# Kernel optimization log

Measured on AMD Instinct MI355X. Metric: run time of the kernel, lower is better.

The kernel has to match this reference:

```python
import jax, jax.numpy as jnp
import numpy as np

B, N = 4, 1024
IN_FEAT = 64
FNET = 64          # code requires fnet_feat == in_feat
OUT_FEAT = 64
RANK = 16
ST1 = 16
ST2 = 16
MIN_NN = 16


def _roll_idx(n_rolls, stride, F):
    # myroll(h, shift) == roll right by `shift` (mod F). Shifts used: 0, then (ss+1)*stride for ss=1..n_rolls-1.
    shifts = np.array([0] + [(ss + 1) * stride for ss in range(1, n_rolls)])
    j = np.arange(F)
    return jnp.asarray((j[None, :] - shifts[:, None]) % F)  # [n_rolls, F]


def setup_inputs() -> dict:
    key = jax.random.key(0)
    ks = jax.random.split(key, 10)
    h = jax.random.normal(ks[0], (B, N, IN_FEAT), jnp.float32)
    D = jax.random.uniform(ks[1], (B, N, N), jnp.float32)
    W0 = jax.random.normal(ks[2], (IN_FEAT, FNET), jnp.float32) * (1.0 / np.sqrt(IN_FEAT))
    b0 = jax.random.normal(ks[3], (1, FNET), jnp.float32) * 0.02
    W1 = jax.random.normal(ks[4], (FNET, ST1 * RANK), jnp.float32) * (1.0 / (np.sqrt(FNET) * np.sqrt(IN_FEAT)))
    b1 = jax.random.normal(ks[5], (1, RANK, IN_FEAT), jnp.float32) * 0.02
    W2 = jax.random.normal(ks[6], (FNET, ST2 * RANK), jnp.float32) * (1.0 / (np.sqrt(FNET) * np.sqrt(IN_FEAT)))
    b2 = jax.random.normal(ks[7], (1, RANK, OUT_FEAT), jnp.float32) * 0.02
    Wl = jax.random.normal(ks[8], (FNET, RANK), jnp.float32) * (1.0 / np.sqrt(RANK))
    bl = jax.random.normal(ks[9], (1, RANK), jnp.float32) * 0.02
    return {"h": h, "D": D, "W0": W0, "b0": b0, "W1": W1, "b1": b1,
            "W2": W2, "b2": b2, "Wl": Wl, "bl": bl}


def reference(h, D, W0, b0, W1, b1, W2, b2, Wl, bl):
    Bb, Nn, f = h.shape
    # k+1 nearest (smallest D): index 0 is the closest ('self'), 1..k are the neighbors
    _, top_idx = jax.lax.top_k(-D, MIN_NN + 1)            # [B, N, K+1]
    top_idx2 = jnp.repeat(top_idx[:, :, 0], MIN_NN, axis=1)  # [B, N*K] (repeat_interleave)
    nbr = top_idx[:, :, 1:].reshape(Bb, Nn * MIN_NN)         # [B, N*K]
    xt1 = jnp.take_along_axis(h, nbr[:, :, None], axis=1)    # [B, N*K, f]
    xt2 = jnp.take_along_axis(h, top_idx2[:, :, None], axis=1)
    labels = (xt1 - xt2).reshape(-1, f)                      # [E, f], E = B*N*K
    x1 = xt1.reshape(-1, f)
    d_labels = jnp.sum(labels * labels, axis=1).reshape(-1, MIN_NN)  # [B*N, K]
    lab = jax.nn.leaky_relu(labels @ W0 + b0, negative_slope=0.02)   # [E, FNET]
    E = lab.shape[0]
    idx1 = _roll_idx(IN_FEAT // ST1, ST1, FNET)
    idx2 = _roll_idx(OUT_FEAT // ST2, ST2, FNET)
    # per-edge weight generation via rolled copies of lab
    theta1 = (lab[:, idx1].reshape(-1, FNET) @ W1).reshape(E, RANK, IN_FEAT) + b1   # [E, R, in]
    theta2 = (lab[:, idx2].reshape(-1, FNET) @ W2).reshape(E, RANK, OUT_FEAT) + b2  # [E, R, out]
    thetal = lab @ Wl + bl                                                          # [E, R]
    x = jnp.einsum('erf,ef->er', theta1, x1) * thetal      # [E, R]
    x = jnp.einsum('ero,er->eo', theta2, x)                # [E, out]
    x = x.reshape(-1, MIN_NN, OUT_FEAT) * jnp.exp(-d_labels / 10.0)[:, :, None]
    x = jnp.sum(x, axis=1).reshape(-1, OUT_FEAT, Nn)       # faithful to torch .reshape(-1, out, N)
    return x
```

## Files before the change

kernel.cpp:

```cpp
#include <hip/hip_runtime.h>
#include <math.h>

#define NN 1024
#define K 16

typedef _Float16 f16;
typedef f16 f16x8 __attribute__((ext_vector_type(8)));
typedef float f32x4 __attribute__((ext_vector_type(4)));

#define W0F_OFF 0
#define W1F_OFF 8192
#define W2F_OFF 40960
#define WLF_OFF 73728
#define B1F_OFF 75776
#define FRAG_BYTES 77824

#define MFMA16(a,b,c) __builtin_amdgcn_mfma_f32_16x16x32_f16((a),(b),(c),0,0,0)

template<int CTRL>
__device__ __forceinline__ float dppf(float v) {
    return __int_as_float(__builtin_amdgcn_update_dpp(0, __float_as_int(v), CTRL, 0xF, 0xF, true));
}
__device__ __forceinline__ float rowsum16(float v) {
    v += dppf<0xB1>(v);
    v += dppf<0x4E>(v);
    v += dppf<0x124>(v);
    v += dppf<0x128>(v);
    return v;
}

__global__ __launch_bounds__(256) void pre_kernel(const float* __restrict__ D,
                                                  const float* __restrict__ W0,
                                                  const float* __restrict__ W1,
                                                  const float* __restrict__ W2,
                                                  const float* __restrict__ Wl,
                                                  const float* __restrict__ b1,
                                                  int* __restrict__ selfIdx,
                                                  int* __restrict__ nbrIdx,
                                                  f16* __restrict__ frag) {
    if (blockIdx.x >= 1024) {
        int c = (blockIdx.x - 1024) * 256 + threadIdx.x;
        if (c >= 76 * 64) return;
        int fg   = c >> 6;
        int lane = c & 63;
        int lrow = lane & 15;
        int kgrp = lane >> 4;
        float src[8];
        if (fg < 8) {
            int kt = fg >> 2, nt = fg & 3;
            int n = nt * 16 + lrow;
#pragma unroll
            for (int i = 0; i < 8; ++i) src[i] = W0[(kt * 32 + kgrp * 8 + i) * 64 + n];
        } else if (fg < 40) {
            int t = fg - 8;
            int q = t >> 3, kt = (t >> 2) & 1, nt = t & 3;
            int f = nt * 16 + lrow;
#pragma unroll
            for (int i = 0; i < 8; ++i) src[i] = W1[f * 256 + q * 64 + kt * 32 + kgrp * 8 + i];
        } else if (fg < 72) {
            int t = fg - 40;
            int q = t >> 3, kt = (t >> 2) & 1, nt = t & 3;
            int o = nt * 16 + lrow;
#pragma unroll
            for (int i = 0; i < 8; ++i) src[i] = W2[(kt * 32 + kgrp * 8 + i) * 256 + q * 64 + o];
        } else if (fg < 74) {
            int kt = fg - 72;
#pragma unroll
            for (int i = 0; i < 8; ++i) src[i] = Wl[(kt * 32 + kgrp * 8 + i) * 16 + lrow];
        } else {
            int kt = fg - 74;
#pragma unroll
            for (int i = 0; i < 8; ++i) src[i] = b1[lrow * 64 + kt * 32 + kgrp * 8 + i];
        }
        f16x8 v;
#pragma unroll
        for (int i = 0; i < 8; ++i) v[i] = (f16)src[i];
        *(f16x8*)((unsigned char*)frag + fg * 1024 + lane * 16) = v;
        return;
    }

    int row  = blockIdx.x * 4 + (threadIdx.x >> 6);
    int lane = threadIdx.x & 63;
    const float* Drow = D + (size_t)row * NN;

    float v[16];
#pragma unroll
    for (int j = 0; j < 16; ++j) v[j] = Drow[j * 64 + lane];

    for (int t = 0; t < K + 1; ++t) {
        float bv = v[0]; int bj = 0;
#pragma unroll
        for (int j = 1; j < 16; ++j)
            if (v[j] < bv) { bv = v[j]; bj = j; }
        int bidx = bj * 64 + lane;
#pragma unroll
        for (int off = 32; off > 0; off >>= 1) {
            float ov = __shfl_xor(bv, off);
            int   oi = __shfl_xor(bidx, off);
            if (ov < bv || (ov == bv && oi < bidx)) { bv = ov; bidx = oi; }
        }
        if (lane == 0) {
            if (t == 0) selfIdx[row] = bidx;
            else        nbrIdx[row * K + (t - 1)] = bidx;
        }
        if ((bidx & 63) == lane) v[bidx >> 6] = INFINITY;
    }
}

__global__ __launch_bounds__(1024, 1) void node_kernel(
    const float* __restrict__ h,
    const float* __restrict__ b0, const float* __restrict__ b2,
    const float* __restrict__ bl,
    const f16* __restrict__ frag,
    const int* __restrict__ selfIdx, const int* __restrict__ nbrIdx,
    float* __restrict__ out) {

    __shared__ __attribute__((aligned(16))) unsigned char sfrag[FRAG_BYTES];
    __shared__ __attribute__((aligned(16))) f16 sbuf[16 * 1152];

    const int tid  = threadIdx.x;
    const int wid  = tid >> 6;
    const int lane = tid & 63;
    const int lrow = lane & 15;
    const int kgrp = lane >> 4;

    {
        const f16x8* gsrc = (const f16x8*)frag;
        f16x8* ldst = (f16x8*)sfrag;
#pragma unroll
        for (int it = 0; it < 5; ++it) {
            int c = tid + it * 1024;
            if (c < FRAG_BYTES / 16) ldst[c] = gsrc[c];
        }
    }
    __syncthreads();

    const unsigned char* fb = sfrag;
    f16* buf = sbuf + wid * 1152;
    const int node = blockIdx.x * 16 + wid;

    const float* hb = h + ((size_t)(node >> 10) << 16);
    const int self = selfIdx[node];
    const int nb   = nbrIdx[node * 16 + lrow];

    f16x8 x1f[2], lrf[2];
    float dp = 0.f;
#pragma unroll
    for (int kt = 0; kt < 2; ++kt) {
        const float* p1 = hb + nb * 64 + kt * 32 + kgrp * 8;
        const float* p2 = hb + self * 64 + kt * 32 + kgrp * 8;
        float4 a0 = *(const float4*)(p1);
        float4 a1 = *(const float4*)(p1 + 4);
        float4 s0 = *(const float4*)(p2);
        float4 s1 = *(const float4*)(p2 + 4);
        float xs[8] = {a0.x,a0.y,a0.z,a0.w,a1.x,a1.y,a1.z,a1.w};
        float ss[8] = {s0.x,s0.y,s0.z,s0.w,s1.x,s1.y,s1.z,s1.w};
#pragma unroll
        for (int i = 0; i < 8; ++i) {
            float t = xs[i] - ss[i];
            x1f[kt][i] = (f16)xs[i];
            lrf[kt][i] = (f16)t;
            dp = fmaf(t, t, dp);
        }
    }
    dp += __shfl_xor(dp, 16);
    dp += __shfl_xor(dp, 32);
    const float dv = dp;

    f32x4 labf[4];
#pragma unroll
    for (int nt = 0; nt < 4; ++nt) {
        float bb = b0[nt * 16 + lrow];
        labf[nt] = (f32x4){bb, bb, bb, bb};
    }
#pragma unroll
    for (int kt = 0; kt < 2; ++kt)
#pragma unroll
        for (int nt = 0; nt < 4; ++nt) {
            f16x8 bf = *(const f16x8*)(fb + W0F_OFF + (kt * 4 + nt) * 1024 + lane * 16);
            labf[nt] = MFMA16(lrf[kt], bf, labf[nt]);
        }
#pragma unroll
    for (int nt = 0; nt < 4; ++nt)
#pragma unroll
        for (int j = 0; j < 4; ++j) {
            float v = labf[nt][j];
            v = v > 0.f ? v : 0.02f * v;
            labf[nt][j] = v;
            buf[(kgrp*4 + j) * 72 + nt*16 + lrow] = (f16)v;
        }

    f32x4 thlf, b1xf;
    {
        float blv = bl[lrow];
        thlf = (f32x4){blv, blv, blv, blv};
        b1xf = (f32x4){0.f, 0.f, 0.f, 0.f};
#pragma unroll
        for (int kt = 0; kt < 2; ++kt) {
            f16x8 wl = *(const f16x8*)(fb + WLF_OFF + kt * 1024 + lane * 16);
            f16x8 bb = *(const f16x8*)(fb + B1F_OFF + kt * 1024 + lane * 16);
            f16x8 la = *(const f16x8*)&buf[lrow * 72 + kt*32 + kgrp*8];
            thlf = MFMA16(la, wl, thlf);
            b1xf = MFMA16(x1f[kt], bb, b1xf);
        }
    }

    f32x4 xof[4];
#pragma unroll
    for (int nt = 0; nt < 4; ++nt) xof[nt] = (f32x4){0.f, 0.f, 0.f, 0.f};

#pragma unroll
    for (int q = 0; q < 4; ++q) {
        f32x4 Uf[4];
#pragma unroll
        for (int nt = 0; nt < 4; ++nt) Uf[nt] = (f32x4){0.f, 0.f, 0.f, 0.f};
#pragma unroll
        for (int kt = 0; kt < 2; ++kt)
#pragma unroll
            for (int nt = 0; nt < 4; ++nt) {
                f16x8 bf = *(const f16x8*)(fb + W1F_OFF + (q*8 + kt*4 + nt) * 1024 + lane * 16);
                Uf[nt] = MFMA16(x1f[kt], bf, Uf[nt]);
            }

        f32x4 dsv[3];
#pragma unroll
        for (int si = 0; si < 3; ++si) {
            const int ts = (si == 0) ? 0 : (si == 1) ? 2 : 3;
            f32x4 p = labf[0] * Uf[(0 + ts) & 3];
            p += labf[1] * Uf[(1 + ts) & 3];
            p += labf[2] * Uf[(2 + ts) & 3];
            p += labf[3] * Uf[(3 + ts) & 3];
#pragma unroll
            for (int j = 0; j < 4; ++j) p[j] = rowsum16(p[j]);
            dsv[si] = p;
        }

        f32x4 xr[4];
#pragma unroll
        for (int p = 0; p < 4; ++p) {
            const int si = (p == 1) ? 1 : (p == 2) ? 2 : 0;
            f32x4 cand = (dsv[si] + b1xf) * thlf;
            int srcl = (lane & 48) | (p * 4 + q);
#pragma unroll
            for (int j = 0; j < 4; ++j) xr[p][j] = __shfl(cand[j], srcl);
        }

        {
            f32x4 x03 = xr[0] + xr[3];
#pragma unroll
            for (int nt = 0; nt < 4; ++nt) {
                f32x4 v = labf[nt] * x03
                        + labf[(nt + 2) & 3] * xr[1]
                        + labf[(nt + 1) & 3] * xr[2];
#pragma unroll
                for (int j = 0; j < 4; ++j)
                    buf[(kgrp*4 + j) * 72 + nt*16 + lrow] = (f16)v[j];
            }
        }

#pragma unroll
        for (int kt = 0; kt < 2; ++kt) {
            f16x8 av = *(const f16x8*)&buf[lrow * 72 + kt*32 + kgrp*8];
#pragma unroll
            for (int nt = 0; nt < 4; ++nt) {
                f16x8 bf = *(const f16x8*)(fb + W2F_OFF + (q*8 + kt*4 + nt) * 1024 + lane * 16);
                xof[nt] = MFMA16(av, bf, xof[nt]);
            }
        }

#pragma unroll
        for (int p = 0; p < 4; ++p)
#pragma unroll
            for (int nt = 0; nt < 4; ++nt) {
                float bv = b2[(p*4 + q) * 64 + nt*16 + lrow];
                xof[nt] += xr[p] * bv;
            }
    }

    f32x4 ew;
#pragma unroll
    for (int j = 0; j < 4; ++j) {
        float dd = __shfl(dv, kgrp * 4 + j);
        ew[j] = __expf(-dd * 0.1f);
    }
    float cs[4];
#pragma unroll
    for (int nt = 0; nt < 4; ++nt) {
        f32x4 wp = xof[nt] * ew;
        float s = wp[0] + wp[1] + wp[2] + wp[3];
        s += __shfl_xor(s, 16);
        s += __shfl_xor(s, 32);
        cs[nt] = s;
    }
    float v = (kgrp == 0) ? cs[0] : (kgrp == 1) ? cs[1] : (kgrp == 2) ? cs[2] : cs[3];
    out[(size_t)node * 64 + lane] = v;
}

extern "C" void kernel_launch(void* const* d_in, const int* in_sizes, int n_in,
                              void* d_out, int out_size, void* d_ws, size_t ws_size,
                              hipStream_t stream) {
    const float* h  = (const float*)d_in[0];
    const float* D  = (const float*)d_in[1];
    const float* W0 = (const float*)d_in[2];
    const float* b0 = (const float*)d_in[3];
    const float* W1 = (const float*)d_in[4];
    const float* b1 = (const float*)d_in[5];
    const float* W2 = (const float*)d_in[6];
    const float* b2 = (const float*)d_in[7];
    const float* Wl = (const float*)d_in[8];
    const float* bl = (const float*)d_in[9];
    float* out = (float*)d_out;

    int* selfIdx = (int*)d_ws;
    int* nbrIdx  = selfIdx + 4096;
    f16* frag    = (f16*)(nbrIdx + 65536);

    pre_kernel<<<1043, 256, 0, stream>>>(D, W0, W1, W2, Wl, b1,
                                         selfIdx, nbrIdx, frag);
    node_kernel<<<256, 1024, 0, stream>>>(h, b0, b2, bl, frag,
                                          selfIdx, nbrIdx, out);
}
```

Measured before the change: 40.52 us.

## Fuse top-k neighbor selection into node kernel and overlap fragment staging

Moves the per-row top-17 search over D from the pre-kernel into the node kernel, so each wave finds its own self and neighbor indices in registers instead of writing them to global memory and reading them back. The weight-fragment global loads are issued into registers before the top-k work and written to shared memory afterward, hiding their latency. The prep kernel now only builds weight fragments with 19 blocks. In exchange, the top-k runs on only 256 blocks of 1024 threads at one block per CU, which lowers parallelism for the D scan.

```diff
diff --git a/kernel.cpp b/kernel.cpp
--- a/kernel.cpp
+++ b/kernel.cpp
@@ -29,90 +29,56 @@
     return v;
 }
 
-__global__ __launch_bounds__(256) void pre_kernel(const float* __restrict__ D,
-                                                  const float* __restrict__ W0,
-                                                  const float* __restrict__ W1,
-                                                  const float* __restrict__ W2,
-                                                  const float* __restrict__ Wl,
-                                                  const float* __restrict__ b1,
-                                                  int* __restrict__ selfIdx,
-                                                  int* __restrict__ nbrIdx,
-                                                  f16* __restrict__ frag) {
-    if (blockIdx.x >= 1024) {
-        int c = (blockIdx.x - 1024) * 256 + threadIdx.x;
-        if (c >= 76 * 64) return;
-        int fg   = c >> 6;
-        int lane = c & 63;
-        int lrow = lane & 15;
-        int kgrp = lane >> 4;
-        float src[8];
-        if (fg < 8) {
-            int kt = fg >> 2, nt = fg & 3;
-            int n = nt * 16 + lrow;
-#pragma unroll
-            for (int i = 0; i < 8; ++i) src[i] = W0[(kt * 32 + kgrp * 8 + i) * 64 + n];
-        } else if (fg < 40) {
-            int t = fg - 8;
-            int q = t >> 3, kt = (t >> 2) & 1, nt = t & 3;
-            int f = nt * 16 + lrow;
-#pragma unroll
-            for (int i = 0; i < 8; ++i) src[i] = W1[f * 256 + q * 64 + kt * 32 + kgrp * 8 + i];
-        } else if (fg < 72) {
-            int t = fg - 40;
-            int q = t >> 3, kt = (t >> 2) & 1, nt = t & 3;
-            int o = nt * 16 + lrow;
-#pragma unroll
-            for (int i = 0; i < 8; ++i) src[i] = W2[(kt * 32 + kgrp * 8 + i) * 256 + q * 64 + o];
-        } else if (fg < 74) {
-            int kt = fg - 72;
-#pragma unroll
-            for (int i = 0; i < 8; ++i) src[i] = Wl[(kt * 32 + kgrp * 8 + i) * 16 + lrow];
-        } else {
-            int kt = fg - 74;
-#pragma unroll
-            for (int i = 0; i < 8; ++i) src[i] = b1[lrow * 64 + kt * 32 + kgrp * 8 + i];
-        }
-        f16x8 v;
-#pragma unroll
-        for (int i = 0; i < 8; ++i) v[i] = (f16)src[i];
-        *(f16x8*)((unsigned char*)frag + fg * 1024 + lane * 16) = v;
-        return;
-    }
-
-    int row  = blockIdx.x * 4 + (threadIdx.x >> 6);
-    int lane = threadIdx.x & 63;
-    const float* Drow = D + (size_t)row * NN;
-
-    float v[16];
-#pragma unroll
-    for (int j = 0; j < 16; ++j) v[j] = Drow[j * 64 + lane];
-
-    for (int t = 0; t < K + 1; ++t) {
-        float bv = v[0]; int bj = 0;
-#pragma unroll
-        for (int j = 1; j < 16; ++j)
-            if (v[j] < bv) { bv = v[j]; bj = j; }
-        int bidx = bj * 64 + lane;
-#pragma unroll
-        for (int off = 32; off > 0; off >>= 1) {
-            float ov = __shfl_xor(bv, off);
-            int   oi = __shfl_xor(bidx, off);
-            if (ov < bv || (ov == bv && oi < bidx)) { bv = ov; bidx = oi; }
-        }
-        if (lane == 0) {
-            if (t == 0) selfIdx[row] = bidx;
-            else        nbrIdx[row * K + (t - 1)] = bidx;
-        }
-        if ((bidx & 63) == lane) v[bidx >> 6] = INFINITY;
-    }
+__global__ __launch_bounds__(256) void prep_kernel(const float* __restrict__ W0,
+                                                   const float* __restrict__ W1,
+                                                   const float* __restrict__ W2,
+                                                   const float* __restrict__ Wl,
+                                                   const float* __restrict__ b1,
+                                                   f16* __restrict__ frag) {
+    int c = blockIdx.x * 256 + threadIdx.x;
+    if (c >= 76 * 64) return;
+    int fg   = c >> 6;
+    int lane = c & 63;
+    int lrow = lane & 15;
+    int kgrp = lane >> 4;
+    float src[8];
+    if (fg < 8) {
+        int kt = fg >> 2, nt = fg & 3;
+        int n = nt * 16 + lrow;
+#pragma unroll
+        for (int i = 0; i < 8; ++i) src[i] = W0[(kt * 32 + kgrp * 8 + i) * 64 + n];
+    } else if (fg < 40) {
+        int t = fg - 8;
+        int q = t >> 3, kt = (t >> 2) & 1, nt = t & 3;
+        int f = nt * 16 + lrow;
+#pragma unroll
+        for (int i = 0; i < 8; ++i) src[i] = W1[f * 256 + q * 64 + kt * 32 + kgrp * 8 + i];
+    } else if (fg < 72) {
+        int t = fg - 40;
+        int q = t >> 3, kt = (t >> 2) & 1, nt = t & 3;
+        int o = nt * 16 + lrow;
+#pragma unroll
+        for (int i = 0; i < 8; ++i) src[i] = W2[(kt * 32 + kgrp * 8 + i) * 256 + q * 64 + o];
+    } else if (fg < 74) {
+        int kt = fg - 72;
+#pragma unroll
+        for (int i = 0; i < 8; ++i) src[i] = Wl[(kt * 32 + kgrp * 8 + i) * 16 + lrow];
+    } else {
+        int kt = fg - 74;
+#pragma unroll
+        for (int i = 0; i < 8; ++i) src[i] = b1[lrow * 64 + kt * 32 + kgrp * 8 + i];
+    }
+    f16x8 v;
+#pragma unroll
+    for (int i = 0; i < 8; ++i) v[i] = (f16)src[i];
+    *(f16x8*)((unsigned char*)frag + fg * 1024 + lane * 16) = v;
 }
 
 __global__ __launch_bounds__(1024, 1) void node_kernel(
-    const float* __restrict__ h,
+    const float* __restrict__ h, const float* __restrict__ D,
     const float* __restrict__ b0, const float* __restrict__ b2,
     const float* __restrict__ bl,
     const f16* __restrict__ frag,
-    const int* __restrict__ selfIdx, const int* __restrict__ nbrIdx,
     float* __restrict__ out) {
 
     __shared__ __attribute__((aligned(16))) unsigned char sfrag[FRAG_BYTES];
@@ -123,25 +89,57 @@
     const int lane = tid & 63;
     const int lrow = lane & 15;
     const int kgrp = lane >> 4;
-
+    const int node = blockIdx.x * 16 + wid;
+
+    f16x8 stg0, stg1, stg2, stg3, stg4;
     {
         const f16x8* gsrc = (const f16x8*)frag;
+        stg0 = gsrc[tid];
+        stg1 = gsrc[tid + 1024];
+        stg2 = gsrc[tid + 2048];
+        stg3 = gsrc[tid + 3072];
+        if (tid < 768) stg4 = gsrc[tid + 4096];
+    }
+
+    int self = 0, nb = 0;
+    {
+        const float* Drow = D + (size_t)node * NN;
+        float v[16];
+#pragma unroll
+        for (int j = 0; j < 16; ++j) v[j] = Drow[j * 64 + lane];
+
+        for (int t = 0; t < K + 1; ++t) {
+            float bv = v[0]; int bj = 0;
+#pragma unroll
+            for (int j = 1; j < 16; ++j)
+                if (v[j] < bv) { bv = v[j]; bj = j; }
+            int bidx = bj * 64 + lane;
+#pragma unroll
+            for (int off = 32; off > 0; off >>= 1) {
+                float ov = __shfl_xor(bv, off);
+                int   oi = __shfl_xor(bidx, off);
+                if (ov < bv || (ov == bv && oi < bidx)) { bv = ov; bidx = oi; }
+            }
+            if (t == 0) self = bidx;
+            else if (lrow == t - 1) nb = bidx;
+            if ((bidx & 63) == lane) v[bidx >> 6] = INFINITY;
+        }
+    }
+
+    {
         f16x8* ldst = (f16x8*)sfrag;
-#pragma unroll
-        for (int it = 0; it < 5; ++it) {
-            int c = tid + it * 1024;
-            if (c < FRAG_BYTES / 16) ldst[c] = gsrc[c];
-        }
+        ldst[tid]        = stg0;
+        ldst[tid + 1024] = stg1;
+        ldst[tid + 2048] = stg2;
+        ldst[tid + 3072] = stg3;
+        if (tid < 768) ldst[tid + 4096] = stg4;
     }
     __syncthreads();
 
     const unsigned char* fb = sfrag;
     f16* buf = sbuf + wid * 1152;
-    const int node = blockIdx.x * 16 + wid;
 
     const float* hb = h + ((size_t)(node >> 10) << 16);
-    const int self = selfIdx[node];
-    const int nb   = nbrIdx[node * 16 + lrow];
 
     f16x8 x1f[2], lrf[2];
     float dp = 0.f;
@@ -311,12 +309,8 @@
     const float* bl = (const float*)d_in[9];
     float* out = (float*)d_out;
 
-    int* selfIdx = (int*)d_ws;
-    int* nbrIdx  = selfIdx + 4096;
-    f16* frag    = (f16*)(nbrIdx + 65536);
-
-    pre_kernel<<<1043, 256, 0, stream>>>(D, W0, W1, W2, Wl, b1,
-                                         selfIdx, nbrIdx, frag);
-    node_kernel<<<256, 1024, 0, stream>>>(h, b0, b2, bl, frag,
-                                          selfIdx, nbrIdx, out);
-}
+    f16* frag = (f16*)d_ws;
+
+    prep_kernel<<<19, 256, 0, stream>>>(W0, W1, W2, Wl, b1, frag);
+    node_kernel<<<256, 1024, 0, stream>>>(h, D, b0, b2, bl, frag, out);
+}
```

Measured after the change: 44.62 us. 1.1x slower.

## Async global-to-LDS weight staging overlapped with gathers; DPP argmin reduction

Applied to the files above, without the earlier changes.

The node kernel now stages the fragment weights into shared memory with global_load_lds direct copies and moves the barrier after the neighbor/self feature gathers, so the weight copy overlaps the h loads. The top-k argmin in pre_kernel replaces four of the six cross-lane shuffles with DPP row operations and uses select-based updates. The launch-bounds min-blocks hint is raised from 1 to 4. The async LDS load needs the barrier to also cover completion of the direct loads (vmcnt), which could be a correctness risk, and the higher occupancy hint may force register limits.

```diff
diff --git a/kernel.cpp b/kernel.cpp
--- a/kernel.cpp
+++ b/kernel.cpp
@@ -7,6 +7,9 @@
 typedef _Float16 f16;
 typedef f16 f16x8 __attribute__((ext_vector_type(8)));
 typedef float f32x4 __attribute__((ext_vector_type(4)));
+
+typedef __attribute__((address_space(1))) void gvoid;
+typedef __attribute__((address_space(3))) void svoid;
 
 #define W0F_OFF 0
 #define W1F_OFF 8192
@@ -21,12 +24,21 @@
 __device__ __forceinline__ float dppf(float v) {
     return __int_as_float(__builtin_amdgcn_update_dpp(0, __float_as_int(v), CTRL, 0xF, 0xF, true));
 }
+template<int CTRL>
+__device__ __forceinline__ int dppi(int v) {
+    return __builtin_amdgcn_update_dpp(0, v, CTRL, 0xF, 0xF, true);
+}
 __device__ __forceinline__ float rowsum16(float v) {
     v += dppf<0xB1>(v);
     v += dppf<0x4E>(v);
     v += dppf<0x124>(v);
     v += dppf<0x128>(v);
     return v;
+}
+__device__ __forceinline__ void argmin_step(float& bv, int& bidx, float ov, int oi) {
+    bool t = (ov < bv) || (ov == bv && oi < bidx);
+    bv = t ? ov : bv;
+    bidx = t ? oi : bidx;
 }
 
 __global__ __launch_bounds__(256) void pre_kernel(const float* __restrict__ D,
@@ -93,12 +105,13 @@
         for (int j = 1; j < 16; ++j)
             if (v[j] < bv) { bv = v[j]; bj = j; }
         int bidx = bj * 64 + lane;
-#pragma unroll
-        for (int off = 32; off > 0; off >>= 1) {
-            float ov = __shfl_xor(bv, off);
-            int   oi = __shfl_xor(bidx, off);
-            if (ov < bv || (ov == bv && oi < bidx)) { bv = ov; bidx = oi; }
-        }
+        argmin_step(bv, bidx, dppf<0xB1>(bv),  dppi<0xB1>(bidx));
+        argmin_step(bv, bidx, dppf<0x4E>(bv),  dppi<0x4E>(bidx));
+        argmin_step(bv, bidx, dppf<0x124>(bv), dppi<0x124>(bidx));
+        argmin_step(bv, bidx, dppf<0x128>(bv), dppi<0x128>(bidx));
+        argmin_step(bv, bidx, __shfl_xor(bv, 16), __shfl_xor(bidx, 16));
+        argmin_step(bv, bidx, __shfl_xor(bv, 32), __shfl_xor(bidx, 32));
+
         if (lane == 0) {
             if (t == 0) selfIdx[row] = bidx;
             else        nbrIdx[row * K + (t - 1)] = bidx;
@@ -107,7 +120,7 @@
     }
 }
 
-__global__ __launch_bounds__(1024, 1) void node_kernel(
+__global__ __launch_bounds__(1024, 4) void node_kernel(
     const float* __restrict__ h,
     const float* __restrict__ b0, const float* __restrict__ b2,
     const float* __restrict__ bl,
@@ -123,25 +136,25 @@
     const int lane = tid & 63;
     const int lrow = lane & 15;
     const int kgrp = lane >> 4;
+    const int node = blockIdx.x * 16 + wid;
 
     {
-        const f16x8* gsrc = (const f16x8*)frag;
-        f16x8* ldst = (f16x8*)sfrag;
+        const unsigned char* gbase = (const unsigned char*)frag;
 #pragma unroll
         for (int it = 0; it < 5; ++it) {
-            int c = tid + it * 1024;
-            if (c < FRAG_BYTES / 16) ldst[c] = gsrc[c];
-        }
-    }
-    __syncthreads();
-
-    const unsigned char* fb = sfrag;
-    f16* buf = sbuf + wid * 1152;
-    const int node = blockIdx.x * 16 + wid;
-
-    const float* hb = h + ((size_t)(node >> 10) << 16);
+            int chunk = it * 1024 + wid * 64;
+            if (chunk < 4864) {
+                __builtin_amdgcn_global_load_lds(
+                    (gvoid*)(gbase + (size_t)(chunk + lane) * 16),
+                    (svoid*)(sfrag + (size_t)chunk * 16),
+                    16, 0, 0);
+            }
+        }
+    }
+
     const int self = selfIdx[node];
     const int nb   = nbrIdx[node * 16 + lrow];
+    const float* hb = h + ((size_t)(node >> 10) << 16);
 
     f16x8 x1f[2], lrf[2];
     float dp = 0.f;
@@ -166,6 +179,11 @@
     dp += __shfl_xor(dp, 16);
     dp += __shfl_xor(dp, 32);
     const float dv = dp;
+
+    __syncthreads();
+
+    const unsigned char* fb = sfrag;
+    f16* buf = sbuf + wid * 1152;
 
     f32x4 labf[4];
 #pragma unroll
```

After: 39.97 us. Within noise of the previous version (-1.3%).
